# Optimization experiments

Hardware: AMD Instinct MI355X
Metric: run time of the kernel (lower is better)

The kernel has to match this reference:

```python
import jax, jax.numpy as jnp
import numpy as np

T_KD = 20.0      # KL_divergence temperature
T_THR = 6.0      # Threshold_weights temperature
EPS = 1e-05


def _margin(o, gathered):
    # torch.sort descending, take top-2; margin only when target is the argmax value
    top2 = jax.lax.top_k(o, 2)[0]                      # [B, 2]
    return jnp.where(top2[:, 0] == gathered, top2[:, 0] - top2[:, 1], 0.0)


def _forward(outputs1, outputs2, outputs3, outputs4, out_s, targets):
    B = targets.shape[0]
    idx = jnp.arange(B)
    mimic = (outputs1 + outputs2 + outputs3 + outputs4) / 4.0

    teachers = [outputs1, outputs2, outputs3, outputs4, mimic]
    gathered = [t[idx, targets] for t in teachers]      # each [B]

    # C = min over gathered target logits of the 4 real teachers
    C = jnp.minimum(jnp.minimum(gathered[0].min(), gathered[1].min()),
                    jnp.minimum(gathered[2].min(), gathered[3].min()))
    # if C < 0: shift everything by (-C + eps); else no shift
    shift = jnp.where(C < 0, -C + EPS, 0.0)

    shifted = [t + shift for t in teachers]
    g_shift = [g + shift for g in gathered]

    # Threshold_weights: margin per branch, softmax over 5 branches
    preds = jnp.stack([_margin(s, g) for s, g in zip(shifted, g_shift)], axis=1)  # [B,5]
    out_threshold = jax.nn.softmax(preds / T_THR, axis=1)

    # max over the 4 (shifted) teacher logit tensors
    max_preds = jnp.maximum(jnp.maximum(shifted[0].max(), shifted[1].max()),
                            jnp.maximum(shifted[2].max(), shifted[3].max()))

    # per-sample CE of student (shared across branches)
    log_p_s = jax.nn.log_softmax(out_s, axis=1)
    CE = -log_p_s[idx, targets]                          # [B]

    log_ps_T = jax.nn.log_softmax(out_s / T_KD, axis=1)  # [B,C]

    def branch_loss(teacher, g_s):
        w2 = g_s / max_preds          # weights2
        w1 = 1.0 - w2                 # weights1
        log_pt = jax.nn.log_softmax(teacher / T_KD, axis=1)
        p_t = jnp.exp(log_pt)
        KD = jnp.sum(p_t * (log_pt - log_ps_T), axis=1) * (T_KD * T_KD)  # [B]
        return w1 * CE + w2 * KD

    # KD/CE use the ORIGINAL (unshifted) teacher logits
    losses = jnp.stack([branch_loss(t, g) for t, g in zip(teachers, g_shift)], axis=1)  # [B,5]
    return jnp.mean(jnp.sum(out_threshold * losses, axis=1))


def setup_inputs() -> dict:
    key = jax.random.key(0)
    ks = jax.random.split(key, 6)
    B, C = 8192, 1000
    return {
        "outputs1": jax.random.normal(ks[0], (B, C), dtype=jnp.float32),
        "outputs2": jax.random.normal(ks[1], (B, C), dtype=jnp.float32),
        "outputs3": jax.random.normal(ks[2], (B, C), dtype=jnp.float32),
        "outputs4": jax.random.normal(ks[3], (B, C), dtype=jnp.float32),
        "out_s": jax.random.normal(ks[4], (B, C), dtype=jnp.float32),
        "targets": jax.random.randint(ks[5], (B,), 0, C, dtype=jnp.int64 if jax.config.jax_enable_x64 else jnp.int32),
    }


def reference(outputs1, outputs2, outputs3, outputs4, out_s, targets):
    return _forward(outputs1, outputs2, outputs3, outputs4, out_s, targets)
```

## Files before the change

### kernel.cpp

```cpp
#include <hip/hip_runtime.h>
#include <math.h>

#define NB 8192
#define NC 1000
#define NF4 250
#define RPB 8


#define LOG2E 1.4426950408889634f
#define LN2   0.6931471805599453f

__device__ __forceinline__ float fexp2(float x) { return __builtin_amdgcn_exp2f(x); }
__device__ __forceinline__ float flog2(float x) { return __builtin_amdgcn_logf(x); }

template <int CTRL>
__device__ __forceinline__ float dpp_mov(float v, float ident) {
  return __uint_as_float((unsigned)__builtin_amdgcn_update_dpp(
      (int)__float_as_uint(ident), (int)__float_as_uint(v), CTRL, 0xF, 0xF,
      false));
}

__device__ __forceinline__ float dppredsum(float v) {
  v += dpp_mov<0x111>(v, 0.f);
  v += dpp_mov<0x112>(v, 0.f);
  v += dpp_mov<0x114>(v, 0.f);
  v += dpp_mov<0x118>(v, 0.f);
  v += dpp_mov<0x142>(v, 0.f);
  v += dpp_mov<0x143>(v, 0.f);
  return v;
}

__device__ __forceinline__ void dppredtop2(float& t1, float& t2) {
  const float NI = -INFINITY;
#define T2STEP(C)                                   \
  {                                                 \
    float i1 = dpp_mov<C>(t1, NI);                  \
    float i2 = dpp_mov<C>(t2, NI);                  \
    t2 = fmaxf(fmaxf(t2, i2), fminf(t1, i1));       \
    t1 = fmaxf(t1, i1);                             \
  }
  T2STEP(0x111) T2STEP(0x112) T2STEP(0x114) T2STEP(0x118)
  T2STEP(0x142) T2STEP(0x143)
#undef T2STEP
}

__device__ __forceinline__ float wredsum(float v) {
#pragma unroll
  for (int m = 32; m >= 1; m >>= 1) v += __shfl_xor(v, m, 64);
  return v;
}
__device__ __forceinline__ float wredmax(float v) {
#pragma unroll
  for (int m = 32; m >= 1; m >>= 1) v = fmaxf(v, __shfl_xor(v, m, 64));
  return v;
}
__device__ __forceinline__ float wredmin(float v) {
#pragma unroll
  for (int m = 32; m >= 1; m >>= 1) v = fminf(v, __shfl_xor(v, m, 64));
  return v;
}
__device__ __forceinline__ float f4get(const float4& v, int e) {
  return e == 0 ? v.x : e == 1 ? v.y : e == 2 ? v.z : v.w;
}

__global__ __launch_bounds__(256) void k_rowstats(
    const float* __restrict__ o1, const float* __restrict__ o2,
    const float* __restrict__ o3, const float* __restrict__ o4,
    const float* __restrict__ os, const int* __restrict__ tg,
    float* __restrict__ ws) {
  const int tid = threadIdx.x;
  const int lane = tid & 63;
  const int wv = tid >> 6;
  const int row0 = blockIdx.x * RPB;
  const int f = (tid < NF4) ? tid : 0;
  const bool act = tid < NF4;
  const float K20 = LOG2E / 20.0f;

  int tgt[RPB];
#pragma unroll
  for (int i = 0; i < RPB; ++i) tgt[i] = tg[row0 + i];

  size_t base = (size_t)row0 * NC;
  float4 c1 = ((const float4*)(o1 + base))[f];
  float4 c2 = ((const float4*)(o2 + base))[f];
  float4 c3 = ((const float4*)(o3 + base))[f];
  float4 c4 = ((const float4*)(o4 + base))[f];
  float4 cs = ((const float4*)(os + base))[f];
  float g1 = 0.f, g2 = 0.f, g3 = 0.f, g4 = 0.f, gs = 0.f;
  if (wv == 0) {
    g1 = o1[base + tgt[0]];
    g2 = o2[base + tgt[0]];
    g3 = o3[base + tgt[0]];
    g4 = o4[base + tgt[0]];
    gs = os[base + tgt[0]];
  }

  __shared__ float sred[4][22];

#pragma unroll 1
  for (int i = 0; i < RPB; ++i) {
    const int row = row0 + i;

    float4 n1, n2, n3, n4, n5;
    float ng1 = 0.f, ng2 = 0.f, ng3 = 0.f, ng4 = 0.f, ng5 = 0.f;
    const bool pf = (i + 1 < RPB);
    if (pf) {
      const size_t nb_ = (size_t)(row + 1) * NC;
      n1 = ((const float4*)(o1 + nb_))[f];
      n2 = ((const float4*)(o2 + nb_))[f];
      n3 = ((const float4*)(o3 + nb_))[f];
      n4 = ((const float4*)(o4 + nb_))[f];
      n5 = ((const float4*)(os + nb_))[f];
      if (wv == 0) {
        ng1 = o1[nb_ + tgt[i + 1]];
        ng2 = o2[nb_ + tgt[i + 1]];
        ng3 = o3[nb_ + tgt[i + 1]];
        ng4 = o4[nb_ + tgt[i + 1]];
        ng5 = os[nb_ + tgt[i + 1]];
      }
    }

    float t1[5], t2[5], Z[5], S1[5];
#pragma unroll
    for (int t = 0; t < 5; ++t) {
      t1[t] = -INFINITY; t2[t] = -INFINITY; Z[t] = 0.f; S1[t] = 0.f;
    }
    float Z1 = 0.f, Z20 = 0.f;

    if (act) {
#pragma unroll
      for (int e = 0; e < 4; ++e) {
        float w0 = f4get(c1, e);
        float w1 = f4get(c2, e);
        float w2 = f4get(c3, e);
        float w3 = f4get(c4, e);
        float wsv = f4get(cs, e);
        float wm = ((w0 + w1) + w2 + w3) * 0.25f;
        float w[5] = {w0, w1, w2, w3, wm};
#pragma unroll
        for (int t = 0; t < 5; ++t) {
          t2[t] = fmaxf(t2[t], fminf(t1[t], w[t]));
          t1[t] = fmaxf(t1[t], w[t]);
          float et = fexp2(w[t] * K20);
          Z[t] += et;
          S1[t] = fmaf(et, w[t] - wsv, S1[t]);
        }
        Z1 += fexp2(wsv * LOG2E);
        Z20 += fexp2(wsv * K20);
      }
    }

#pragma unroll
    for (int t = 0; t < 5; ++t) dppredtop2(t1[t], t2[t]);
#pragma unroll
    for (int t = 0; t < 5; ++t) { Z[t] = dppredsum(Z[t]); S1[t] = dppredsum(S1[t]); }
    Z1 = dppredsum(Z1);
    Z20 = dppredsum(Z20);

    if (lane == 63) {
#pragma unroll
      for (int t = 0; t < 5; ++t) {
        sred[wv][t] = t1[t];
        sred[wv][5 + t] = t2[t];
        sred[wv][10 + t] = Z[t];
        sred[wv][15 + t] = S1[t];
      }
      sred[wv][20] = Z1;
      sred[wv][21] = Z20;
    }
    __syncthreads();

    if (tid == 0) {
      float T1[5], T2[5], ZZ[5], SS[5], z1, z20;
#pragma unroll
      for (int t = 0; t < 5; ++t) {
        T1[t] = sred[0][t]; T2[t] = sred[0][5 + t];
        ZZ[t] = sred[0][10 + t]; SS[t] = sred[0][15 + t];
      }
      z1 = sred[0][20]; z20 = sred[0][21];
#pragma unroll
      for (int w = 1; w < 4; ++w) {
#pragma unroll
        for (int t = 0; t < 5; ++t) {
          float a1 = sred[w][t], a2 = sred[w][5 + t];
          float lo = fminf(T1[t], a1);
          T1[t] = fmaxf(T1[t], a1);
          T2[t] = fmaxf(fmaxf(T2[t], a2), lo);
          ZZ[t] += sred[w][10 + t];
          SS[t] += sred[w][15 + t];
        }
        z1 += sred[w][20];
        z20 += sred[w][21];
      }

      const float gm = ((g1 + g2) + g3 + g4) * 0.25f;
      float gg[5] = {g1, g2, g3, g4, gm};

      const float lse_s = flog2(z20) * LN2;
      const float CE = flog2(z1) * LN2 - gs;

#pragma unroll
      for (int t = 0; t < 5; ++t) {
        float lse_t = flog2(ZZ[t]) * LN2;
        float KD = 400.0f * (SS[t] / (20.0f * ZZ[t]) - lse_t + lse_s);
        float margin = (T1[t] == gg[t]) ? (T1[t] - T2[t]) : 0.0f;
        ws[(size_t)t * NB + row] = margin;
        ws[(size_t)(5 + t) * NB + row] = gg[t];
        ws[(size_t)(10 + t) * NB + row] = KD;
      }
      ws[(size_t)15 * NB + row] = CE;
      ws[(size_t)16 * NB + row] = fminf(fminf(g1, g2), fminf(g3, g4));
      ws[(size_t)17 * NB + row] = fmaxf(fmaxf(T1[0], T1[1]), fmaxf(T1[2], T1[3]));
    }
    __syncthreads();

    if (pf) {
      c1 = n1; c2 = n2; c3 = n3; c4 = n4; cs = n5;
      g1 = ng1; g2 = ng2; g3 = ng3; g4 = ng4; gs = ng5;
    }
  }
}

__global__ __launch_bounds__(1024) void k_minmax(float* __restrict__ ws,
                                                 float* __restrict__ out) {
  const int tid = threadIdx.x;
  const int lane = tid & 63, wv = tid >> 6;
  __shared__ float sA[16], sB[16];

  float mn = INFINITY, mx = -INFINITY;
  for (int r = tid; r < NB; r += 1024) {
    mn = fminf(mn, ws[(size_t)16 * NB + r]);
    mx = fmaxf(mx, ws[(size_t)17 * NB + r]);
  }
  mn = wredmin(mn);
  mx = wredmax(mx);
  if (lane == 0) { sA[wv] = mn; sB[wv] = mx; }
  __syncthreads();
  if (tid == 0) {
    float a = sA[0], b = sB[0];
    for (int i = 1; i < 16; ++i) { a = fminf(a, sA[i]); b = fmaxf(b, sB[i]); }
    float shift = (a < 0.0f) ? (-a + 1e-5f) : 0.0f;
    ws[(size_t)18 * NB] = shift;
    ws[(size_t)18 * NB + 1] = b + shift;
    out[0] = 0.0f;
  }
}

__global__ __launch_bounds__(256) void k_loss(const float* __restrict__ ws,
                                              float* __restrict__ out) {
  const int tid = threadIdx.x;
  const int lane = tid & 63, wv = tid >> 6;
  const int r = blockIdx.x * 256 + tid;
  __shared__ float sA[4];

  const float shift = ws[(size_t)18 * NB];
  const float maxp = ws[(size_t)18 * NB + 1];
  const float K6 = LOG2E / 6.0f;

  float m[5], e[5];
#pragma unroll
  for (int t = 0; t < 5; ++t) m[t] = ws[(size_t)t * NB + r];
  float pm = fmaxf(fmaxf(fmaxf(m[0], m[1]), fmaxf(m[2], m[3])), m[4]);
  float Zl = 0.0f;
#pragma unroll
  for (int t = 0; t < 5; ++t) { e[t] = fexp2((m[t] - pm) * K6); Zl += e[t]; }
  float ce = ws[(size_t)15 * NB + r];
  float rl = 0.0f;
#pragma unroll
  for (int t = 0; t < 5; ++t) {
    float g = ws[(size_t)(5 + t) * NB + r];
    float kd = ws[(size_t)(10 + t) * NB + r];
    float w2 = (g + shift) / maxp;
    float loss = (1.0f - w2) * ce + w2 * kd;
    rl += e[t] * loss;
  }
  float acc = rl / Zl;

  acc = wredsum(acc);
  if (lane == 0) sA[wv] = acc;
  __syncthreads();
  if (tid == 0) {
    float tot = (sA[0] + sA[1]) + (sA[2] + sA[3]);
    atomicAdd(out, tot * (1.0f / 8192.0f));
  }
}

extern "C" void kernel_launch(void* const* d_in, const int* in_sizes, int n_in,
                              void* d_out, int out_size, void* d_ws, size_t ws_size,
                              hipStream_t stream) {
  const float* o1 = (const float*)d_in[0];
  const float* o2 = (const float*)d_in[1];
  const float* o3 = (const float*)d_in[2];
  const float* o4 = (const float*)d_in[3];
  const float* os = (const float*)d_in[4];
  const int* tg = (const int*)d_in[5];
  float* ws = (float*)d_ws;
  float* out = (float*)d_out;

  k_rowstats<<<NB / RPB, 256, 0, stream>>>(o1, o2, o3, o4, os, tg, ws);
  k_minmax<<<1, 1024, 0, stream>>>(ws, out);
  k_loss<<<NB / 256, 256, 0, stream>>>(ws, out);
}
```

Baseline: 200.0 us.

## Remove per-row block barriers by writing per-wave partials and combining in new kernel

The row-stats kernel no longer reduces the four wave partials through shared memory with two __syncthreads per row. Each wave now writes its partial top-2, sum and entropy values to a global workspace, and a new k_combine kernel merges them per row and computes margin, KD and CE. Rows per block also drop from 8 to 4, which doubles the grid. This removes barrier stalls and serial tid==0 work in the streaming kernel, at the cost of an extra launch and roughly 93 floats per row of extra global traffic.

```diff
diff --git a/kernel.cpp b/kernel.cpp
--- a/kernel.cpp
+++ b/kernel.cpp
@@ -4,7 +4,7 @@
 #define NB 8192
 #define NC 1000
 #define NF4 250
-#define RPB 8
+#define RPB 4
 
 
 #define LOG2E 1.4426950408889634f
@@ -75,6 +75,7 @@
   const int f = (tid < NF4) ? tid : 0;
   const bool act = tid < NF4;
   const float K20 = LOG2E / 20.0f;
+  float* __restrict__ w2p = ws + (size_t)19 * NB;
 
   int tgt[RPB];
 #pragma unroll
@@ -94,8 +95,6 @@
     g4 = o4[base + tgt[0]];
     gs = os[base + tgt[0]];
   }
-
-  __shared__ float sred[4][22];
 
 #pragma unroll 1
   for (int i = 0; i < RPB; ++i) {
@@ -160,65 +159,79 @@
     if (lane == 63) {
 #pragma unroll
       for (int t = 0; t < 5; ++t) {
-        sred[wv][t] = t1[t];
-        sred[wv][5 + t] = t2[t];
-        sred[wv][10 + t] = Z[t];
-        sred[wv][15 + t] = S1[t];
+        w2p[(size_t)(wv * 22 + t) * NB + row] = t1[t];
+        w2p[(size_t)(wv * 22 + 5 + t) * NB + row] = t2[t];
+        w2p[(size_t)(wv * 22 + 10 + t) * NB + row] = Z[t];
+        w2p[(size_t)(wv * 22 + 15 + t) * NB + row] = S1[t];
       }
-      sred[wv][20] = Z1;
-      sred[wv][21] = Z20;
-    }
-    __syncthreads();
-
-    if (tid == 0) {
-      float T1[5], T2[5], ZZ[5], SS[5], z1, z20;
-#pragma unroll
-      for (int t = 0; t < 5; ++t) {
-        T1[t] = sred[0][t]; T2[t] = sred[0][5 + t];
-        ZZ[t] = sred[0][10 + t]; SS[t] = sred[0][15 + t];
+      w2p[(size_t)(wv * 22 + 20) * NB + row] = Z1;
+      w2p[(size_t)(wv * 22 + 21) * NB + row] = Z20;
+      if (wv == 0) {
+        w2p[(size_t)88 * NB + row] = g1;
+        w2p[(size_t)89 * NB + row] = g2;
+        w2p[(size_t)90 * NB + row] = g3;
+        w2p[(size_t)91 * NB + row] = g4;
+        w2p[(size_t)92 * NB + row] = gs;
       }
-      z1 = sred[0][20]; z20 = sred[0][21];
-#pragma unroll
-      for (int w = 1; w < 4; ++w) {
-#pragma unroll
-        for (int t = 0; t < 5; ++t) {
-          float a1 = sred[w][t], a2 = sred[w][5 + t];
-          float lo = fminf(T1[t], a1);
-          T1[t] = fmaxf(T1[t], a1);
-          T2[t] = fmaxf(fmaxf(T2[t], a2), lo);
-          ZZ[t] += sred[w][10 + t];
-          SS[t] += sred[w][15 + t];
-        }
-        z1 += sred[w][20];
-        z20 += sred[w][21];
-      }
-
-      const float gm = ((g1 + g2) + g3 + g4) * 0.25f;
-      float gg[5] = {g1, g2, g3, g4, gm};
-
-      const float lse_s = flog2(z20) * LN2;
-      const float CE = flog2(z1) * LN2 - gs;
-
-#pragma unroll
-      for (int t = 0; t < 5; ++t) {
-        float lse_t = flog2(ZZ[t]) * LN2;
-        float KD = 400.0f * (SS[t] / (20.0f * ZZ[t]) - lse_t + lse_s);
-        float margin = (T1[t] == gg[t]) ? (T1[t] - T2[t]) : 0.0f;
-        ws[(size_t)t * NB + row] = margin;
-        ws[(size_t)(5 + t) * NB + row] = gg[t];
-        ws[(size_t)(10 + t) * NB + row] = KD;
-      }
-      ws[(size_t)15 * NB + row] = CE;
-      ws[(size_t)16 * NB + row] = fminf(fminf(g1, g2), fminf(g3, g4));
-      ws[(size_t)17 * NB + row] = fmaxf(fmaxf(T1[0], T1[1]), fmaxf(T1[2], T1[3]));
-    }
-    __syncthreads();
+    }
 
     if (pf) {
       c1 = n1; c2 = n2; c3 = n3; c4 = n4; cs = n5;
       g1 = ng1; g2 = ng2; g3 = ng3; g4 = ng4; gs = ng5;
     }
   }
+}
+
+__global__ __launch_bounds__(256) void k_combine(float* __restrict__ ws) {
+  const int row = blockIdx.x * 256 + threadIdx.x;
+  const float* __restrict__ w2p = ws + (size_t)19 * NB;
+
+  float T1[5], T2[5], ZZ[5], SS[5];
+#pragma unroll
+  for (int t = 0; t < 5; ++t) {
+    T1[t] = -INFINITY; T2[t] = -INFINITY; ZZ[t] = 0.f; SS[t] = 0.f;
+  }
+  float z1 = 0.f, z20 = 0.f;
+
+#pragma unroll
+  for (int s = 0; s < 4; ++s) {
+#pragma unroll
+    for (int t = 0; t < 5; ++t) {
+      float a1 = w2p[(size_t)(s * 22 + t) * NB + row];
+      float a2 = w2p[(size_t)(s * 22 + 5 + t) * NB + row];
+      float lo = fminf(T1[t], a1);
+      T1[t] = fmaxf(T1[t], a1);
+      T2[t] = fmaxf(fmaxf(T2[t], a2), lo);
+      ZZ[t] += w2p[(size_t)(s * 22 + 10 + t) * NB + row];
+      SS[t] += w2p[(size_t)(s * 22 + 15 + t) * NB + row];
+    }
+    z1 += w2p[(size_t)(s * 22 + 20) * NB + row];
+    z20 += w2p[(size_t)(s * 22 + 21) * NB + row];
+  }
+
+  const float g1 = w2p[(size_t)88 * NB + row];
+  const float g2 = w2p[(size_t)89 * NB + row];
+  const float g3 = w2p[(size_t)90 * NB + row];
+  const float g4 = w2p[(size_t)91 * NB + row];
+  const float gs = w2p[(size_t)92 * NB + row];
+  const float gm = ((g1 + g2) + g3 + g4) * 0.25f;
+  float gg[5] = {g1, g2, g3, g4, gm};
+
+  const float lse_s = flog2(z20) * LN2;
+  const float CE = flog2(z1) * LN2 - gs;
+
+#pragma unroll
+  for (int t = 0; t < 5; ++t) {
+    float lse_t = flog2(ZZ[t]) * LN2;
+    float KD = 400.0f * (SS[t] / (20.0f * ZZ[t]) - lse_t + lse_s);
+    float margin = (T1[t] == gg[t]) ? (T1[t] - T2[t]) : 0.0f;
+    ws[(size_t)t * NB + row] = margin;
+    ws[(size_t)(5 + t) * NB + row] = gg[t];
+    ws[(size_t)(10 + t) * NB + row] = KD;
+  }
+  ws[(size_t)15 * NB + row] = CE;
+  ws[(size_t)16 * NB + row] = fminf(fminf(g1, g2), fminf(g3, g4));
+  ws[(size_t)17 * NB + row] = fmaxf(fmaxf(T1[0], T1[1]), fmaxf(T1[2], T1[3]));
 }
 
 __global__ __launch_bounds__(1024) void k_minmax(float* __restrict__ ws,
@@ -298,6 +311,7 @@
   float* out = (float*)d_out;
 
   k_rowstats<<<NB / RPB, 256, 0, stream>>>(o1, o2, o3, o4, os, tg, ws);
+  k_combine<<<NB / 256, 256, 0, stream>>>(ws);
   k_minmax<<<1, 1024, 0, stream>>>(ws, out);
   k_loss<<<NB / 256, 256, 0, stream>>>(ws, out);
 }
```

New measurement: 200.9 us. No clear change (+0.4%).
